# Optimization experiments

Hardware: AMD Instinct MI355X
Metric: run time of the kernel (lower is better)

The kernel has to match this reference:

```python
import jax, jax.numpy as jnp
import numpy as np

B = 4096          # batch
N_ENT = 200000    # n_entities
N_USR = 50000
N_REL = 32
K = 64            # neighbors per entity
D2 = 128          # dim*2
EPS = 1e-5


def setup_inputs() -> dict:
    key = jax.random.key(0)
    ks = jax.random.split(key, 10)
    return {
        "u": jax.random.randint(ks[0], (B,), 0, N_USR),
        "i": jax.random.randint(ks[1], (B,), 0, N_ENT),
        "adj_entity": jax.random.randint(ks[2], (N_ENT, K), 0, N_ENT),
        "adj_relation": jax.random.randint(ks[3], (N_ENT, K), 0, N_REL),
        "entity_embs": jax.random.normal(ks[4], (N_ENT, D2), jnp.float32),
        "relation_embs": jax.random.normal(ks[5], (N_REL, D2), jnp.float32),
        "bn_gamma": jnp.ones((D2,), jnp.float32),
        "bn_beta": jnp.zeros((D2,), jnp.float32),
        "bn_mean": jnp.zeros((D2,), jnp.float32),
        "bn_var": jnp.ones((D2,), jnp.float32),
        "Wr1_w": jax.random.normal(ks[6], (D2, D2), jnp.float32) * 0.05,
        "Wr1_b": jnp.zeros((D2,), jnp.float32),
        "W1_w": jax.random.normal(ks[7], (D2, D2), jnp.float32) * 0.05,
        "W1_b": jnp.zeros((D2,), jnp.float32),
        "wl_w": jax.random.normal(ks[8], (2 * D2, 1), jnp.float32) * 0.05,
        "wl_b": jnp.zeros((1,), jnp.float32),
    }


def reference(u, i, adj_entity, adj_relation, entity_embs, relation_embs,
              bn_gamma, bn_beta, bn_mean, bn_var,
              Wr1_w, Wr1_b, W1_w, W1_b, wl_w, wl_b):
    # eval mode: all dropout / edge-drop are identity, BN uses running stats
    def bn(x):
        return (x - bn_mean) * bn_gamma * jax.lax.rsqrt(bn_var + EPS) + bn_beta

    def lrelu(x):
        return jnp.where(x >= 0, x, 0.2 * x)

    def layer(h, idx):
        t = entity_embs[adj_entity[idx]]        # [B, K, D2] neighbor gather
        r = relation_embs[adj_relation[idx]]    # [B, K, D2]
        tr = t @ Wr1_w + Wr1_b                  # Wr1(t)
        hr = jnp.tanh((h @ Wr1_w + Wr1_b)[:, None, :] + r)
        hrt = hr * tr                           # [B, K, D2]
        s = jnp.sum(hrt, axis=1)
        Nh = s * s - jnp.sum(hrt * hrt, axis=1)  # FM: sq-of-sum - sum-of-sq
        out = lrelu((h + Nh) @ W1_w + W1_b)      # agg_method='other'
        return h + out

    u_e = bn(entity_embs[u])
    h = bn(entity_embs[i])
    # n_layers = 1
    h = layer(h, i)
    u_e = layer(u_e, u)
    combined = jnp.concatenate([u_e, h], axis=-1)  # [B, 2*D2]
    return (combined @ wl_w + wl_b)[:, 0]
```

## Files before the change

### kernel.cpp

```cpp
#include <hip/hip_runtime.h>

#define B     4096
#define KNB   64
#define D     128
#define NREL  32
#define EPS   1e-5f

typedef __attribute__((ext_vector_type(8))) short bf16x8;
typedef __attribute__((ext_vector_type(4))) float f32x4;

__device__ inline unsigned short f2bf(float f) {
    unsigned u = __float_as_uint(f);
    return (unsigned short)((u + 0x7FFFu + ((u >> 16) & 1u)) >> 16);
}
__device__ inline unsigned cvt_pk_bf16(float lo, float hi) {
    unsigned r;
    asm("v_cvt_pk_bf16_f32 %0, %1, %2" : "=v"(r) : "v"(lo), "v"(hi));
    return r;
}
__device__ inline unsigned short cvt1_bf16(float f) {
    return (unsigned short)(cvt_pk_bf16(f, f) & 0xFFFFu);
}
__device__ inline float bfu_lo(unsigned u) { return __uint_as_float(u << 16); }
__device__ inline float bfu_hi(unsigned u) { return __uint_as_float(u & 0xFFFF0000u); }

__device__ inline float fast_tanh(float x) {
    float e = __builtin_amdgcn_exp2f(x * 2.885390082f);
    return 1.f - 2.f * __builtin_amdgcn_rcpf(e + 1.f);
}

__global__ __launch_bounds__(256) void prep(
    const int* __restrict__ i_idx, const int* __restrict__ u_idx,
    const float* __restrict__ embs,
    const float* __restrict__ gamma, const float* __restrict__ beta,
    const float* __restrict__ mean,  const float* __restrict__ var,
    float* __restrict__ h0,
    const float* __restrict__ W, unsigned short* __restrict__ Wt)
{
    const int t = threadIdx.x;
    if (blockIdx.x == 1024) {
        #pragma unroll
        for (int m = 0; m < 64; ++m) {
            const int idx = m * 256 + t;
            const int k = idx >> 7, n = idx & 127;
            Wt[n * D + k] = f2bf(W[idx]);
        }
        return;
    }
    const int tid = blockIdx.x * 256 + t;
    const int d4 = tid & 31;
    const int b  = (tid >> 5) & (B - 1);
    const int j  = tid >> 17;
    const int idx = j ? u_idx[b] : i_idx[b];

    const int d0 = d4 * 4;
    float4 x = *(const float4*)&embs[(size_t)idx * D + d0];
    float4 m = *(const float4*)&mean[d0];
    float4 v = *(const float4*)&var[d0];
    float4 g = *(const float4*)&gamma[d0];
    float4 bt = *(const float4*)&beta[d0];

    float4 o;
    o.x = (x.x - m.x) * g.x * rsqrtf(v.x + EPS) + bt.x;
    o.y = (x.y - m.y) * g.y * rsqrtf(v.y + EPS) + bt.y;
    o.z = (x.z - m.z) * g.z * rsqrtf(v.z + EPS) + bt.z;
    o.w = (x.w - m.w) * g.w * rsqrtf(v.w + EPS) + bt.w;

    *(float4*)&h0[(size_t)tid * 4] = o;
}

__global__ __launch_bounds__(256) void gemm_etr(
    const float* __restrict__ in, const unsigned short* __restrict__ Wt,
    const float* __restrict__ bias, unsigned short* __restrict__ outbf,
    const float* __restrict__ in2, float* __restrict__ out2, int nb1)
{
    __shared__ unsigned short Al[64 * 128];
    __shared__ unsigned short Wl[128 * 128];

    const int t = threadIdx.x;
    const bool second = (int)blockIdx.x >= nb1;
    const float* src = second ? in2 : in;
    const size_t row0 = (size_t)(second ? (int)blockIdx.x - nb1 : (int)blockIdx.x) * 64;

    {
        const float4* w4 = (const float4*)Wt;
        #pragma unroll
        for (int m = 0; m < 8; ++m) {
            const int c = m * 256 + t;
            const int n = c >> 4;
            float4 v = w4[c];
            *(float4*)((char*)Wl + ((c * 16) ^ ((n & 7) << 4))) = v;
        }
    }
    {
        #pragma unroll
        for (int m = 0; m < 4; ++m) {
            const int c = m * 256 + t;
            const int r = c >> 4;
            const int k0 = (c & 15) * 8;
            const float4* s = (const float4*)&src[(row0 + r) * D + k0];
            const float4 x = s[0], y = s[1];
            uint4 h;
            h.x = cvt_pk_bf16(x.x, x.y);
            h.y = cvt_pk_bf16(x.z, x.w);
            h.z = cvt_pk_bf16(y.x, y.y);
            h.w = cvt_pk_bf16(y.z, y.w);
            *(uint4*)((char*)Al + ((r * 256 + k0 * 2) ^ ((r & 7) << 4))) = h;
        }
    }
    __syncthreads();

    const int wv   = t >> 6;
    const int lane = t & 63;
    const int rw   = wv * 16;
    const int lrow = lane & 15;
    const int kgrp = lane >> 4;

    f32x4 acc[8];
    #pragma unroll
    for (int n = 0; n < 8; ++n) acc[n] = (f32x4){0.f, 0.f, 0.f, 0.f};

    #pragma unroll
    for (int ks = 0; ks < 4; ++ks) {
        const int arow = rw + lrow;
        const bf16x8 a = *(const bf16x8*)((const char*)Al +
            ((arow * 256 + ks * 64 + kgrp * 16) ^ ((arow & 7) << 4)));
        #pragma unroll
        for (int n = 0; n < 8; ++n) {
            const int brow = n * 16 + lrow;
            const bf16x8 b = *(const bf16x8*)((const char*)Wl +
                ((brow * 256 + ks * 64 + kgrp * 16) ^ ((brow & 7) << 4)));
            acc[n] = __builtin_amdgcn_mfma_f32_16x16x32_bf16(a, b, acc[n], 0, 0, 0);
        }
    }

    if (second) {
        #pragma unroll
        for (int n = 0; n < 8; ++n) {
            const float bv = bias[n * 16 + lrow];
            #pragma unroll
            for (int i = 0; i < 4; ++i) {
                const size_t r = row0 + rw + kgrp * 4 + i;
                out2[r * D + n * 16 + lrow] = acc[n][i] + bv;
            }
        }
        return;
    }

    __syncthreads();
    #pragma unroll
    for (int n = 0; n < 8; ++n) {
        const float bv = bias[n * 16 + lrow];
        #pragma unroll
        for (int i = 0; i < 4; ++i) {
            const int r = rw + kgrp * 4 + i;
            const int cb = (r * 256 + (n * 16 + lrow) * 2) ^ ((r & 7) << 4);
            *(unsigned short*)((char*)Al + cb) = cvt1_bf16(acc[n][i] + bv);
        }
    }
    __syncthreads();
    {
        float4* dst = (float4*)(outbf + row0 * D);
        #pragma unroll
        for (int m = 0; m < 4; ++m) {
            const int c = m * 256 + t;
            const int r = c >> 4;
            dst[c] = *(const float4*)((const char*)Al + ((c * 16) ^ ((r & 7) << 4)));
        }
    }
}

__global__ __launch_bounds__(256) void aggregate(
    const int* __restrict__ i_idx, const int* __restrict__ u_idx,
    const int* __restrict__ adj_e, const int* __restrict__ adj_r,
    const unsigned short* __restrict__ Etr, const float* __restrict__ rel_embs,
    const float* __restrict__ hW,  const float* __restrict__ h0,
    float* __restrict__ g_out)
{
    __shared__ float tt[NREL * D];
    __shared__ int ents[KNB];
    __shared__ int rels[KNB];
    __shared__ float ps[4][D];
    __shared__ float pq[4][D];

    const int t = threadIdx.x;
    const int b = blockIdx.x & (B - 1);
    const int j = blockIdx.x >> 12;
    const size_t rowbase = ((size_t)j * B + b) * D;
    const int idx = j ? u_idx[b] : i_idx[b];

    const float4 hv = *(const float4*)&hW[rowbase + (t & 31) * 4];

    if (t < KNB) {
        ents[t] = adj_e[(size_t)idx * KNB + t] * (D * 2);
        rels[t] = adj_r[(size_t)idx * KNB + t] * (D * 4);
    }
    __syncthreads();

    const int dq  = t & 31;
    const int grp = t >> 5;
    const char* Eb = (const char*)Etr + dq * 8;
    const char* tb = (const char*)tt  + dq * 16;

    uint2 ev[8];
    int rk[8];
    #pragma unroll
    for (int it = 0; it < 8; ++it) {
        const int k = grp + it * 8;
        ev[it] = *(const uint2*)(Eb + ents[k]);
        rk[it] = rels[k];
    }

    {
        const float4* re4 = (const float4*)rel_embs;
        #pragma unroll
        for (int c = 0; c < 4; ++c) {
            const int m4 = t + c * 256;
            const float4 r = re4[m4];
            float4 o;
            o.x = fast_tanh(hv.x + r.x);
            o.y = fast_tanh(hv.y + r.y);
            o.z = fast_tanh(hv.z + r.z);
            o.w = fast_tanh(hv.w + r.w);
            *(float4*)&tt[m4 * 4] = o;
        }
    }
    __syncthreads();

    float s0 = 0.f, s1 = 0.f, s2 = 0.f, s3 = 0.f;
    float q0 = 0.f, q1 = 0.f, q2 = 0.f, q3 = 0.f;
    #pragma unroll
    for (int it = 0; it < 8; ++it) {
        const float4 tv = *(const float4*)(tb + rk[it]);
        const float v0 = bfu_lo(ev[it].x) * tv.x;
        const float v1 = bfu_hi(ev[it].x) * tv.y;
        const float v2 = bfu_lo(ev[it].y) * tv.z;
        const float v3 = bfu_hi(ev[it].y) * tv.w;
        s0 += v0; s1 += v1; s2 += v2; s3 += v3;
        q0 = fmaf(v0, v0, q0); q1 = fmaf(v1, v1, q1);
        q2 = fmaf(v2, v2, q2); q3 = fmaf(v3, v3, q3);
    }
    s0 += __shfl_xor(s0, 32); s1 += __shfl_xor(s1, 32);
    s2 += __shfl_xor(s2, 32); s3 += __shfl_xor(s3, 32);
    q0 += __shfl_xor(q0, 32); q1 += __shfl_xor(q1, 32);
    q2 += __shfl_xor(q2, 32); q3 += __shfl_xor(q3, 32);

    const int wv = t >> 6;
    if ((t & 63) < 32) {
        *(float4*)&ps[wv][dq * 4] = make_float4(s0, s1, s2, s3);
        *(float4*)&pq[wv][dq * 4] = make_float4(q0, q1, q2, q3);
    }
    __syncthreads();

    if (t < D) {
        const float ss = ps[0][t] + ps[1][t] + ps[2][t] + ps[3][t];
        const float qq = pq[0][t] + pq[1][t] + pq[2][t] + pq[3][t];
        g_out[rowbase + t] = h0[rowbase + t] + ss * ss - qq;
    }
}

__global__ __launch_bounds__(256) void gemm_fin(
    const float* __restrict__ gb, const float* __restrict__ W,
    const float* __restrict__ bias, const float* __restrict__ h0,
    const float* __restrict__ wl_w, const float* __restrict__ wl_b,
    float* __restrict__ out)
{
    __shared__ float Wl[128 * 128];
    __shared__ float inl[32 * 128];
    __shared__ float rowdot[32];
    const int t = threadIdx.x;
    const int b0 = blockIdx.x * 16;

    {
        const float4* W4 = (const float4*)W;
        float4* Wl4 = (float4*)Wl;
        #pragma unroll
        for (int m = 0; m < 16; ++m) Wl4[t + m * 256] = W4[t + m * 256];
    }
    {
        const float4* gb4 = (const float4*)gb;
        float4* inl4 = (float4*)inl;
        #pragma unroll
        for (int m = 0; m < 4; ++m) {
            const int c = m * 256 + t;
            const int r = c >> 5;
            const size_t grow = (r < 16) ? (size_t)(b0 + r) : (size_t)(B + b0 + r - 16);
            inl4[c] = gb4[grow * 32 + (c & 31)];
        }
    }
    __syncthreads();

    const int c0 = (t & 31) * 4;
    const int r0 = (t >> 5) * 4;

    float acc[4][4];
    {
        float4 bv = *(const float4*)&bias[c0];
        #pragma unroll
        for (int i = 0; i < 4; ++i) {
            acc[i][0] = bv.x; acc[i][1] = bv.y; acc[i][2] = bv.z; acc[i][3] = bv.w;
        }
    }

    for (int k = 0; k < 128; k += 4) {
        float4 a[4], w[4];
        #pragma unroll
        for (int i = 0; i < 4; ++i) a[i] = *(const float4*)&inl[(r0 + i) * D + k];
        #pragma unroll
        for (int kk = 0; kk < 4; ++kk) w[kk] = *(const float4*)&Wl[(k + kk) * D + c0];
        #pragma unroll
        for (int i = 0; i < 4; ++i) {
            const float* ai = (const float*)&a[i];
            #pragma unroll
            for (int kk = 0; kk < 4; ++kk) {
                acc[i][0] = fmaf(ai[kk], w[kk].x, acc[i][0]);
                acc[i][1] = fmaf(ai[kk], w[kk].y, acc[i][1]);
                acc[i][2] = fmaf(ai[kk], w[kk].z, acc[i][2]);
                acc[i][3] = fmaf(ai[kk], w[kk].w, acc[i][3]);
            }
        }
    }

    const int seg = (r0 < 16) ? 128 : 0;
    const float4 wv = *(const float4*)&wl_w[seg + c0];
    float pr[4];
    #pragma unroll
    for (int i = 0; i < 4; ++i) {
        const int r = r0 + i;
        const size_t grow = (r < 16) ? (size_t)(b0 + r) : (size_t)(B + b0 + r - 16);
        const float4 ad = *(const float4*)&h0[grow * D + c0];
        float4 o;
        o.x = ad.x + (acc[i][0] >= 0.f ? acc[i][0] : 0.2f * acc[i][0]);
        o.y = ad.y + (acc[i][1] >= 0.f ? acc[i][1] : 0.2f * acc[i][1]);
        o.z = ad.z + (acc[i][2] >= 0.f ? acc[i][2] : 0.2f * acc[i][2]);
        o.w = ad.w + (acc[i][3] >= 0.f ? acc[i][3] : 0.2f * acc[i][3]);
        pr[i] = o.x * wv.x + o.y * wv.y + o.z * wv.z + o.w * wv.w;
    }
    #pragma unroll
    for (int off = 1; off <= 16; off <<= 1) {
        pr[0] += __shfl_xor(pr[0], off);
        pr[1] += __shfl_xor(pr[1], off);
        pr[2] += __shfl_xor(pr[2], off);
        pr[3] += __shfl_xor(pr[3], off);
    }
    if ((t & 31) == 0) {
        rowdot[r0]     = pr[0];
        rowdot[r0 + 1] = pr[1];
        rowdot[r0 + 2] = pr[2];
        rowdot[r0 + 3] = pr[3];
    }
    __syncthreads();
    if (t < 16) out[b0 + t] = wl_b[0] + rowdot[t + 16] + rowdot[t];
}

extern "C" void kernel_launch(void* const* d_in, const int* in_sizes, int n_in,
                              void* d_out, int out_size, void* d_ws, size_t ws_size,
                              hipStream_t stream) {
    const int*   u        = (const int*)d_in[0];
    const int*   ii       = (const int*)d_in[1];
    const int*   adj_e    = (const int*)d_in[2];
    const int*   adj_r    = (const int*)d_in[3];
    const float* embs     = (const float*)d_in[4];
    const float* rel_embs = (const float*)d_in[5];
    const float* gamma    = (const float*)d_in[6];
    const float* beta     = (const float*)d_in[7];
    const float* mean     = (const float*)d_in[8];
    const float* var      = (const float*)d_in[9];
    const float* Wr1_w    = (const float*)d_in[10];
    const float* Wr1_b    = (const float*)d_in[11];
    const float* W1_w     = (const float*)d_in[12];
    const float* W1_b     = (const float*)d_in[13];
    const float* wl_w     = (const float*)d_in[14];
    const float* wl_b     = (const float*)d_in[15];
    float* out = (float*)d_out;

    const int n_ent = in_sizes[2] / KNB;
    const int nb1 = n_ent / 64;

    char* p = (char*)d_ws;
    unsigned short* Etr = (unsigned short*)p;           p += (size_t)n_ent * D * 2;
    unsigned short* Wt  = (unsigned short*)p;           p += (size_t)D * D * 2;
    float* h0   = (float*)p;                            p += (size_t)2 * B * D * 4;
    float* hWb  = (float*)p;                            p += (size_t)2 * B * D * 4;
    float* gb   = (float*)p;

    prep<<<1025, 256, 0, stream>>>(ii, u, embs, gamma, beta, mean, var, h0, Wr1_w, Wt);
    gemm_etr<<<nb1 + (2 * B) / 64, 256, 0, stream>>>(embs, Wt, Wr1_b, Etr, h0, hWb, nb1);
    aggregate<<<2 * B, 256, 0, stream>>>(ii, u, adj_e, adj_r, Etr, rel_embs, hWb, h0, gb);
    gemm_fin<<<B / 16, 256, 0, stream>>>(gb, W1_w, W1_b, h0, wl_w, wl_b, out);
}
```

Measured before the change: 78.64 us.

## Fuse batch-norm gather into GEMM and cut aggregate LDS and register use

The batch-norm of the gathered user and item embeddings moves out of the 1025-block prep kernel and into the second half of gemm_etr. prep now only converts the weight and precomputes per-channel scale and shift. This drops one full pass that wrote h0 and then read it back before the GEMM. In aggregate, the partial-sum buffers now reuse the tanh table LDS (guarded by an extra barrier), the relation offsets are reread from LDS instead of held in registers, h0 is loaded early, and a launch-bounds occupancy hint of 6 is added.

```diff
diff --git a/kernel.cpp b/kernel.cpp
--- a/kernel.cpp
+++ b/kernel.cpp
@@ -30,56 +30,37 @@
 }
 
 __global__ __launch_bounds__(256) void prep(
-    const int* __restrict__ i_idx, const int* __restrict__ u_idx,
-    const float* __restrict__ embs,
+    const float* __restrict__ W, unsigned short* __restrict__ Wt,
     const float* __restrict__ gamma, const float* __restrict__ beta,
     const float* __restrict__ mean,  const float* __restrict__ var,
-    float* __restrict__ h0,
-    const float* __restrict__ W, unsigned short* __restrict__ Wt)
+    float* __restrict__ scale, float* __restrict__ shift)
 {
     const int t = threadIdx.x;
-    if (blockIdx.x == 1024) {
-        #pragma unroll
-        for (int m = 0; m < 64; ++m) {
-            const int idx = m * 256 + t;
-            const int k = idx >> 7, n = idx & 127;
-            Wt[n * D + k] = f2bf(W[idx]);
-        }
-        return;
-    }
-    const int tid = blockIdx.x * 256 + t;
-    const int d4 = tid & 31;
-    const int b  = (tid >> 5) & (B - 1);
-    const int j  = tid >> 17;
-    const int idx = j ? u_idx[b] : i_idx[b];
-
-    const int d0 = d4 * 4;
-    float4 x = *(const float4*)&embs[(size_t)idx * D + d0];
-    float4 m = *(const float4*)&mean[d0];
-    float4 v = *(const float4*)&var[d0];
-    float4 g = *(const float4*)&gamma[d0];
-    float4 bt = *(const float4*)&beta[d0];
-
-    float4 o;
-    o.x = (x.x - m.x) * g.x * rsqrtf(v.x + EPS) + bt.x;
-    o.y = (x.y - m.y) * g.y * rsqrtf(v.y + EPS) + bt.y;
-    o.z = (x.z - m.z) * g.z * rsqrtf(v.z + EPS) + bt.z;
-    o.w = (x.w - m.w) * g.w * rsqrtf(v.w + EPS) + bt.w;
-
-    *(float4*)&h0[(size_t)tid * 4] = o;
+    #pragma unroll
+    for (int m = 0; m < 64; ++m) {
+        const int idx = m * 256 + t;
+        const int k = idx >> 7, n = idx & 127;
+        Wt[n * D + k] = f2bf(W[idx]);
+    }
+    if (t < D) {
+        const float sc = gamma[t] * rsqrtf(var[t] + EPS);
+        scale[t] = sc;
+        shift[t] = beta[t] - mean[t] * sc;
+    }
 }
 
 __global__ __launch_bounds__(256) void gemm_etr(
-    const float* __restrict__ in, const unsigned short* __restrict__ Wt,
+    const float* __restrict__ embs, const unsigned short* __restrict__ Wt,
     const float* __restrict__ bias, unsigned short* __restrict__ outbf,
-    const float* __restrict__ in2, float* __restrict__ out2, int nb1)
+    const int* __restrict__ i_idx, const int* __restrict__ u_idx,
+    const float* __restrict__ scale, const float* __restrict__ shift,
+    float* __restrict__ h0out, float* __restrict__ out2, int nb1)
 {
     __shared__ unsigned short Al[64 * 128];
     __shared__ unsigned short Wl[128 * 128];
 
     const int t = threadIdx.x;
     const bool second = (int)blockIdx.x >= nb1;
-    const float* src = second ? in2 : in;
     const size_t row0 = (size_t)(second ? (int)blockIdx.x - nb1 : (int)blockIdx.x) * 64;
 
     {
@@ -92,13 +73,13 @@
             *(float4*)((char*)Wl + ((c * 16) ^ ((n & 7) << 4))) = v;
         }
     }
-    {
+    if (!second) {
         #pragma unroll
         for (int m = 0; m < 4; ++m) {
             const int c = m * 256 + t;
             const int r = c >> 4;
             const int k0 = (c & 15) * 8;
-            const float4* s = (const float4*)&src[(row0 + r) * D + k0];
+            const float4* s = (const float4*)&embs[(row0 + r) * D + k0];
             const float4 x = s[0], y = s[1];
             uint4 h;
             h.x = cvt_pk_bf16(x.x, x.y);
@@ -107,6 +88,35 @@
             h.w = cvt_pk_bf16(y.z, y.w);
             *(uint4*)((char*)Al + ((r * 256 + k0 * 2) ^ ((r & 7) << 4))) = h;
         }
+    } else {
+        #pragma unroll
+        for (int m = 0; m < 4; ++m) {
+            const int c = m * 256 + t;
+            const int r = c >> 4;
+            const int k0 = (c & 15) * 8;
+            const int grow = (int)row0 + r;
+            const int bb = grow & (B - 1);
+            const int idxv = (grow >= B) ? u_idx[bb] : i_idx[bb];
+            const float4* s = (const float4*)&embs[(size_t)idxv * D + k0];
+            const float4 x = s[0], y = s[1];
+            const float4 sc0 = *(const float4*)&scale[k0];
+            const float4 sc1 = *(const float4*)&scale[k0 + 4];
+            const float4 sh0 = *(const float4*)&shift[k0];
+            const float4 sh1 = *(const float4*)&shift[k0 + 4];
+            float4 a0, a1;
+            a0.x = fmaf(x.x, sc0.x, sh0.x); a0.y = fmaf(x.y, sc0.y, sh0.y);
+            a0.z = fmaf(x.z, sc0.z, sh0.z); a0.w = fmaf(x.w, sc0.w, sh0.w);
+            a1.x = fmaf(y.x, sc1.x, sh1.x); a1.y = fmaf(y.y, sc1.y, sh1.y);
+            a1.z = fmaf(y.z, sc1.z, sh1.z); a1.w = fmaf(y.w, sc1.w, sh1.w);
+            *(float4*)&h0out[(size_t)grow * D + k0]     = a0;
+            *(float4*)&h0out[(size_t)grow * D + k0 + 4] = a1;
+            uint4 h;
+            h.x = cvt_pk_bf16(a0.x, a0.y);
+            h.y = cvt_pk_bf16(a0.z, a0.w);
+            h.z = cvt_pk_bf16(a1.x, a1.y);
+            h.w = cvt_pk_bf16(a1.z, a1.w);
+            *(uint4*)((char*)Al + ((r * 256 + k0 * 2) ^ ((r & 7) << 4))) = h;
+        }
     }
     __syncthreads();
 
@@ -170,7 +180,7 @@
     }
 }
 
-__global__ __launch_bounds__(256) void aggregate(
+__global__ __launch_bounds__(256, 6) void aggregate(
     const int* __restrict__ i_idx, const int* __restrict__ u_idx,
     const int* __restrict__ adj_e, const int* __restrict__ adj_r,
     const unsigned short* __restrict__ Etr, const float* __restrict__ rel_embs,
@@ -180,8 +190,8 @@
     __shared__ float tt[NREL * D];
     __shared__ int ents[KNB];
     __shared__ int rels[KNB];
-    __shared__ float ps[4][D];
-    __shared__ float pq[4][D];
+    float* ps = tt;
+    float* pq = tt + 4 * D;
 
     const int t = threadIdx.x;
     const int b = blockIdx.x & (B - 1);
@@ -190,6 +200,8 @@
     const int idx = j ? u_idx[b] : i_idx[b];
 
     const float4 hv = *(const float4*)&hW[rowbase + (t & 31) * 4];
+    float h0v = 0.f;
+    if (t < D) h0v = h0[rowbase + t];
 
     if (t < KNB) {
         ents[t] = adj_e[(size_t)idx * KNB + t] * (D * 2);
@@ -203,13 +215,9 @@
     const char* tb = (const char*)tt  + dq * 16;
 
     uint2 ev[8];
-    int rk[8];
-    #pragma unroll
-    for (int it = 0; it < 8; ++it) {
-        const int k = grp + it * 8;
-        ev[it] = *(const uint2*)(Eb + ents[k]);
-        rk[it] = rels[k];
-    }
+    #pragma unroll
+    for (int it = 0; it < 8; ++it)
+        ev[it] = *(const uint2*)(Eb + ents[grp + it * 8]);
 
     {
         const float4* re4 = (const float4*)rel_embs;
@@ -231,7 +239,7 @@
     float q0 = 0.f, q1 = 0.f, q2 = 0.f, q3 = 0.f;
     #pragma unroll
     for (int it = 0; it < 8; ++it) {
-        const float4 tv = *(const float4*)(tb + rk[it]);
+        const float4 tv = *(const float4*)(tb + rels[grp + it * 8]);
         const float v0 = bfu_lo(ev[it].x) * tv.x;
         const float v1 = bfu_hi(ev[it].x) * tv.y;
         const float v2 = bfu_lo(ev[it].y) * tv.z;
@@ -245,17 +253,19 @@
     q0 += __shfl_xor(q0, 32); q1 += __shfl_xor(q1, 32);
     q2 += __shfl_xor(q2, 32); q3 += __shfl_xor(q3, 32);
 
+    __syncthreads();
+
     const int wv = t >> 6;
     if ((t & 63) < 32) {
-        *(float4*)&ps[wv][dq * 4] = make_float4(s0, s1, s2, s3);
-        *(float4*)&pq[wv][dq * 4] = make_float4(q0, q1, q2, q3);
+        *(float4*)&ps[wv * D + dq * 4] = make_float4(s0, s1, s2, s3);
+        *(float4*)&pq[wv * D + dq * 4] = make_float4(q0, q1, q2, q3);
     }
     __syncthreads();
 
     if (t < D) {
-        const float ss = ps[0][t] + ps[1][t] + ps[2][t] + ps[3][t];
-        const float qq = pq[0][t] + pq[1][t] + pq[2][t] + pq[3][t];
-        g_out[rowbase + t] = h0[rowbase + t] + ss * ss - qq;
+        const float ss = ps[t] + ps[D + t] + ps[2 * D + t] + ps[3 * D + t];
+        const float qq = pq[t] + pq[D + t] + pq[2 * D + t] + pq[3 * D + t];
+        g_out[rowbase + t] = h0v + ss * ss - qq;
     }
 }
 
@@ -380,12 +390,15 @@
     char* p = (char*)d_ws;
     unsigned short* Etr = (unsigned short*)p;           p += (size_t)n_ent * D * 2;
     unsigned short* Wt  = (unsigned short*)p;           p += (size_t)D * D * 2;
+    float* scale = (float*)p;                           p += D * 4;
+    float* shift = (float*)p;                           p += D * 4;
     float* h0   = (float*)p;                            p += (size_t)2 * B * D * 4;
     float* hWb  = (float*)p;                            p += (size_t)2 * B * D * 4;
     float* gb   = (float*)p;
 
-    prep<<<1025, 256, 0, stream>>>(ii, u, embs, gamma, beta, mean, var, h0, Wr1_w, Wt);
-    gemm_etr<<<nb1 + (2 * B) / 64, 256, 0, stream>>>(embs, Wt, Wr1_b, Etr, h0, hWb, nb1);
+    prep<<<1, 256, 0, stream>>>(Wr1_w, Wt, gamma, beta, mean, var, scale, shift);
+    gemm_etr<<<nb1 + (2 * B) / 64, 256, 0, stream>>>(embs, Wt, Wr1_b, Etr,
+                                                     ii, u, scale, shift, h0, hWb, nb1);
     aggregate<<<2 * B, 256, 0, stream>>>(ii, u, adj_e, adj_r, Etr, rel_embs, hWb, h0, gb);
     gemm_fin<<<B / 16, 256, 0, stream>>>(gb, W1_w, W1_b, h0, wl_w, wl_b, out);
 }
```

Result: no change. 79.75 us (+1.4%).
